# Kernel tuning notes

Measured on AMD Instinct MI355X. Metric: run time of the kernel, lower is better.

The kernel has to match this reference:

```python
import jax, jax.numpy as jnp
import numpy as np

B, L, D, H = 2, 1024, 512, 8
h = D // H            # head_dim = 64
K = H                 # num_eigh must equal num_heads (vmap pairing in conv)
EPS = 1e-5


def _spectral_filters(seq_len: int, k: int) -> np.ndarray:
    # Hankel matrix Z_{ij} = 2 / ((i+j)^3 - (i+j)), top-k eigenvectors scaled by sigma^{1/4}
    e = np.arange(1, seq_len + 1, dtype=np.float64)
    ipj = e[:, None] + e[None, :]
    Z = 2.0 / (ipj ** 3 - ipj)
    sigma, phi = np.linalg.eigh(Z)
    sigma_k = np.clip(sigma[-k:], 1e-9, None)
    return (phi[:, -k:] * sigma_k ** 0.25).astype(np.float32)  # [L, K]


def setup_inputs() -> dict:
    key = jax.random.key(0)
    ks = jax.random.split(key, 8)
    s = 0.02
    return {
        "x": jax.random.normal(ks[0], (B, L, D), jnp.float32),
        "spectral_basis": jnp.asarray(_spectral_filters(L, K)),       # [L, K]
        "wq_w": jax.random.normal(ks[1], (D, D), jnp.float32) * s,
        "wq_b": jnp.zeros((D,), jnp.float32),
        "wk_w": jax.random.normal(ks[2], (D, D), jnp.float32) * s,
        "wk_b": jnp.zeros((D,), jnp.float32),
        "wv_w": jax.random.normal(ks[3], (D, D), jnp.float32) * s,
        "wv_b": jnp.zeros((D,), jnp.float32),
        "wo_w": jax.random.normal(ks[4], (D, D), jnp.float32) * s,
        "wo_b": jnp.zeros((D,), jnp.float32),
        "wg_w": jax.random.normal(ks[5], (h * h,), jnp.float32) * s,  # Linear(h^2 -> 1)
        "wg_b": jnp.zeros((), jnp.float32),
    }


def _causal_fft_conv(u, filt_f, n):
    # u: [B,H,L,h]; filt_f: precomputed rfft of per-head filters [H, F]
    Uf = jnp.fft.rfft(u, n=n, axis=2)                        # [B,H,F,h]
    y = jnp.fft.irfft(Uf * filt_f[None, :, :, None], n=n, axis=2)
    return y[:, :, :L]                                       # truncate full conv -> causal


def reference(x, spectral_basis, wq_w, wq_b, wk_w, wk_b, wv_w, wv_b,
              wo_w, wo_b, wg_w, wg_b):
    # projections -> [B,H,L,h]
    q = (x @ wq_w + wq_b).reshape(B, L, H, h).transpose(0, 2, 1, 3)
    k = (x @ wk_w + wk_b).reshape(B, L, H, h).transpose(0, 2, 1, 3) * h ** (-0.5)
    v = (x @ wv_w + wv_b).reshape(B, L, H, h).transpose(0, 2, 1, 3)

    n = 2 * L
    filt_f = jnp.fft.rfft(spectral_basis.T, n=n, axis=1)     # [H, F] (one filter per head)
    k_conv = _causal_fft_conv(k, filt_f, n)
    v_conv = _causal_fft_conv(v, filt_f, n)

    # gated outer product Z: [B,H,L,h,h]
    Z = jnp.einsum('bhlm,bhln->bhlmn', v_conv, k_conv)
    gate_logits = Z.reshape(B, H, L, h * h) @ wg_w + wg_b    # [B,H,L]
    gates = jax.nn.relu(gate_logits) ** 2 + EPS
    gated_Z = gates[..., None, None] * Z

    # associative scan (additive) over sequence dim
    cumul_gated_Z = jnp.cumsum(gated_Z, axis=2)              # [B,H,L,h,h]
    cumul_gates = jnp.cumsum(gates, axis=2)                  # [B,H,L]
    attn = cumul_gated_Z / (cumul_gates[..., None, None] + EPS)

    # note: original einsum sums over l (and d) independently of s
    ctxt = jnp.einsum('bhsd,bhlde->bhse', q, attn)           # [B,H,L,h]
    norm = jnp.linalg.norm(ctxt, axis=3, keepdims=True)
    unit = ctxt / jnp.maximum(norm, EPS)                     # F.normalize semantics
    out = unit.transpose(0, 2, 1, 3).reshape(B, L, D)
    return out @ wo_w + wo_b
```

## Files before the change

### kernel.cpp

```cpp
#include <hip/hip_runtime.h>
#include <math.h>


typedef __attribute__((ext_vector_type(8))) short short8;
typedef __attribute__((ext_vector_type(4))) float floatx4;

__device__ __forceinline__ unsigned short f2bf(float f) {
    unsigned int u = __float_as_uint(f);
    unsigned int r = (u + 0x7FFFu + ((u >> 16) & 1u)) >> 16;
    return (unsigned short)r;
}

__global__ __launch_bounds__(256) void k_prep(
    const float* __restrict__ x,
    const float* __restrict__ wq, const float* __restrict__ wk,
    const float* __restrict__ wv, const float* __restrict__ wo,
    const float* __restrict__ wg,
    unsigned short* __restrict__ xb,
    unsigned short* __restrict__ wT, unsigned short* __restrict__ woT,
    unsigned short* __restrict__ wgb)
{
    __shared__ float sf[64][65];
    const int blk = blockIdx.x;
    const int tid = threadIdx.x;

    if (blk < 512) {
        const int gid = blk * 256 + tid;
        const float4* x4 = (const float4*)x;
        float4 a = x4[gid*2], b = x4[gid*2+1];
        uint4 o;
        o.x = f2bf(a.x) | ((unsigned)f2bf(a.y) << 16);
        o.y = f2bf(a.z) | ((unsigned)f2bf(a.w) << 16);
        o.z = f2bf(b.x) | ((unsigned)f2bf(b.y) << 16);
        o.w = f2bf(b.z) | ((unsigned)f2bf(b.w) << 16);
        ((uint4*)xb)[gid] = o;
    } else if (blk < 768) {
        const int t = blk - 512;
        const float* src; unsigned short* dst; int n0, c0, k0;
        if (t < 192) {
            int nt = t >> 3, kt = t & 7;
            n0 = nt * 64; k0 = kt * 64;
            int z = n0 >> 9; c0 = n0 & 511;
            src = (z == 0) ? wq : (z == 1) ? wk : wv;
            dst = wT;
        } else {
            int u = t - 192; int nt = u >> 3, kt = u & 7;
            n0 = nt * 64; c0 = n0; k0 = kt * 64;
            src = wo; dst = woT;
        }
        const int rr = tid >> 4, c4 = tid & 15;
        #pragma unroll
        for (int g = 0; g < 4; ++g) {
            int r = g*16 + rr;
            float4 v = *(const float4*)&src[(size_t)(k0 + r)*512 + c0 + c4*4];
            sf[r][c4*4+0]=v.x; sf[r][c4*4+1]=v.y; sf[r][c4*4+2]=v.z; sf[r][c4*4+3]=v.w;
        }
        __syncthreads();
        #pragma unroll
        for (int g = 0; g < 4; ++g) {
            int c = g*16 + rr;
            int kk = c4*4;
            ushort4 o;
            o.x = f2bf(sf[kk+0][c]); o.y = f2bf(sf[kk+1][c]);
            o.z = f2bf(sf[kk+2][c]); o.w = f2bf(sf[kk+3][c]);
            *(ushort4*)&dst[(size_t)(n0 + c)*512 + k0 + kk] = o;
        }
    } else {
        const float4* wg4 = (const float4*)wg;
        for (int i = tid; i < 512; i += 256) {
            float4 a = wg4[i*2], b = wg4[i*2+1];
            uint4 o;
            o.x = f2bf(a.x) | ((unsigned)f2bf(a.y) << 16);
            o.y = f2bf(a.z) | ((unsigned)f2bf(a.w) << 16);
            o.z = f2bf(b.x) | ((unsigned)f2bf(b.y) << 16);
            o.w = f2bf(b.z) | ((unsigned)f2bf(b.w) << 16);
            ((uint4*)wgb)[i] = o;
        }
    }
}

__global__ __launch_bounds__(256) void k_qkv_mfma(
    const unsigned short* __restrict__ xb, const unsigned short* __restrict__ wT,
    const float* __restrict__ bq, const float* __restrict__ bk,
    const float* __restrict__ bv,
    float* __restrict__ qo, unsigned short* __restrict__ ub2)
{
    const int tid = threadIdx.x;
    const int lane = tid & 63, wave = tid >> 6;
    const int q = lane >> 4, ln = lane & 15;
    const int wm = wave * 32;
    const int m0 = blockIdx.y * 128;
    const int n0 = blockIdx.x * 64;

    __shared__ unsigned short As[128*72];
    __shared__ unsigned short Bs[64*72];

    floatx4 acc[2][4];
    #pragma unroll
    for (int i = 0; i < 2; ++i)
        #pragma unroll
        for (int j = 0; j < 4; ++j)
            acc[i][j] = (floatx4){0.f, 0.f, 0.f, 0.f};

    const uint4* Ag = (const uint4*)xb;
    const uint4* Bg = (const uint4*)wT;
    for (int k0 = 0; k0 < 512; k0 += 64) {
        #pragma unroll
        for (int s = 0; s < 4; ++s) {
            int idx = s*256 + tid;
            int r = idx >> 3, cp = idx & 7;
            uint4 va = Ag[(size_t)(m0 + r)*64 + (k0 >> 3) + cp];
            *(uint4*)&As[r*72 + cp*8] = va;
        }
        #pragma unroll
        for (int s = 0; s < 2; ++s) {
            int idx = s*256 + tid;
            int r = idx >> 3, cp = idx & 7;
            uint4 vb = Bg[(size_t)(n0 + r)*64 + (k0 >> 3) + cp];
            *(uint4*)&Bs[r*72 + cp*8] = vb;
        }
        __syncthreads();
        short8 af0[2], af1[2], bf0[4], bf1[4];
        #pragma unroll
        for (int i = 0; i < 2; ++i) {
            af0[i] = *(const short8*)&As[(wm + i*16 + ln)*72 + q*8];
            af1[i] = *(const short8*)&As[(wm + i*16 + ln)*72 + 32 + q*8];
        }
        #pragma unroll
        for (int i = 0; i < 4; ++i) {
            bf0[i] = *(const short8*)&Bs[(i*16 + ln)*72 + q*8];
            bf1[i] = *(const short8*)&Bs[(i*16 + ln)*72 + 32 + q*8];
        }
        #pragma unroll
        for (int mi = 0; mi < 2; ++mi)
            #pragma unroll
            for (int ni = 0; ni < 4; ++ni) {
                acc[mi][ni] = __builtin_amdgcn_mfma_f32_16x16x32_bf16(
                    af0[mi], bf0[ni], acc[mi][ni], 0, 0, 0);
                acc[mi][ni] = __builtin_amdgcn_mfma_f32_16x16x32_bf16(
                    af1[mi], bf1[ni], acc[mi][ni], 0, 0, 0);
            }
        __syncthreads();
    }

    const int z = n0 >> 9;
    if (z == 0) {
        #pragma unroll
        for (int mi = 0; mi < 2; ++mi) {
            #pragma unroll
            for (int ni = 0; ni < 4; ++ni) {
                int c = (n0 + ni*16 + ln) & 511;
                int head = c >> 6, dd = c & 63;
                float bb = bq[c];
                #pragma unroll
                for (int reg = 0; reg < 4; ++reg) {
                    int row = m0 + wm + mi*16 + q*4 + reg;
                    int b = row >> 10, l = row & 1023;
                    qo[(size_t)((b*8 + head)*1024 + l)*64 + dd] =
                        acc[mi][ni][reg] + bb;
                }
            }
        }
    } else {
        const float scale = (z == 1) ? 0.125f : 1.0f;
        const float* bias = (z == 1) ? bk : bv;
        unsigned short* dst = ub2 + (size_t)(z-1) * 16 * 64 * 1024;
        #pragma unroll
        for (int mi = 0; mi < 2; ++mi) {
            #pragma unroll
            for (int ni = 0; ni < 4; ++ni) {
                int c = (n0 + ni*16 + ln) & 511;
                int head = c >> 6, dd = c & 63;
                float bb = bias[c];
                int row0 = m0 + wm + mi*16 + q*4;
                int b = row0 >> 10, l0 = row0 & 1023;
                ushort4 o;
                o.x = f2bf((acc[mi][ni][0] + bb) * scale);
                o.y = f2bf((acc[mi][ni][1] + bb) * scale);
                o.z = f2bf((acc[mi][ni][2] + bb) * scale);
                o.w = f2bf((acc[mi][ni][3] + bb) * scale);
                *(ushort4*)&dst[((size_t)((b*8 + head)*64) + dd)*1024 + l0] = o;
            }
        }
    }
}

__global__ __launch_bounds__(256) void k_conv_gate(
    const float* __restrict__ sb,
    const unsigned short* __restrict__ ub2,
    const unsigned short* __restrict__ wgb, const float* __restrict__ wg_b,
    float* __restrict__ kc, float* __restrict__ vc,
    float* __restrict__ gl)
{
    const int tid = threadIdx.x;
    const int lane = tid & 63, wave = tid >> 6;
    const int q = lane >> 4, ln = lane & 15;
    const int bh  = blockIdx.x, h = bh & 7;
    const int it  = blockIdx.y;
    const int t0  = it * 64;

    __shared__ unsigned short revf[1152];
    __shared__ unsigned short Bk[64*72];
    __shared__ unsigned short Bv[64*72];

    for (int i = tid; i < 1152; i += 256) {
        int d = 1087 - i;
        revf[i] = (d >= 0 && d < 1024) ? f2bf(sb[d*8 + h]) : (unsigned short)0;
    }

    const uint4* Bg = (const uint4*)ub2;
    const size_t bk_base = (size_t)bh * 8192;
    const size_t bv_base = (size_t)(16 + bh) * 8192;

    floatx4 acck[4], accv[4];
    #pragma unroll
    for (int i = 0; i < 4; ++i) {
        acck[i] = (floatx4){0.f,0.f,0.f,0.f};
        accv[i] = (floatx4){0.f,0.f,0.f,0.f};
    }

    const int kend = t0 + 64;
    const int arow = 1087 - t0 - (wave*16 + ln);
    for (int k0 = 0; k0 < kend; k0 += 64) {
        #pragma unroll
        for (int s = 0; s < 2; ++s) {
            int idx = s*256 + tid;
            int r = idx >> 3, cp = idx & 7;
            *(uint4*)&Bk[r*72 + cp*8] = Bg[bk_base + (size_t)r*128 + (k0 >> 3) + cp];
            *(uint4*)&Bv[r*72 + cp*8] = Bg[bv_base + (size_t)r*128 + (k0 >> 3) + cp];
        }
        __syncthreads();
        const int ab = arow + k0 + q*8;
        short8 a0, a1;
        #pragma unroll
        for (int j = 0; j < 8; ++j) {
            a0[j] = (short)revf[ab + j];
            a1[j] = (short)revf[ab + 32 + j];
        }
        #pragma unroll
        for (int ni = 0; ni < 4; ++ni) {
            short8 kb0 = *(const short8*)&Bk[(ni*16 + ln)*72 + q*8];
            short8 kb1 = *(const short8*)&Bk[(ni*16 + ln)*72 + 32 + q*8];
            short8 vb0 = *(const short8*)&Bv[(ni*16 + ln)*72 + q*8];
            short8 vb1 = *(const short8*)&Bv[(ni*16 + ln)*72 + 32 + q*8];
            acck[ni] = __builtin_amdgcn_mfma_f32_16x16x32_bf16(a0, kb0, acck[ni], 0, 0, 0);
            acck[ni] = __builtin_amdgcn_mfma_f32_16x16x32_bf16(a1, kb1, acck[ni], 0, 0, 0);
            accv[ni] = __builtin_amdgcn_mfma_f32_16x16x32_bf16(a0, vb0, accv[ni], 0, 0, 0);
            accv[ni] = __builtin_amdgcn_mfma_f32_16x16x32_bf16(a1, vb1, accv[ni], 0, 0, 0);
        }
        __syncthreads();
    }

    float* kdst = kc + (size_t)bh * 65536;
    float* vdst = vc + (size_t)bh * 65536;
    #pragma unroll
    for (int ni = 0; ni < 4; ++ni)
        #pragma unroll
        for (int reg = 0; reg < 4; ++reg) {
            int row = wave*16 + q*4 + reg;
            int grow = t0 + row;
            kdst[(size_t)grow*64 + ni*16 + ln] = acck[ni][reg];
            vdst[(size_t)grow*64 + ni*16 + ln] = accv[ni][reg];
            Bk[row*72 + ni*16 + ln] = f2bf(acck[ni][reg]);
        }
    {
        const uint4* Wg = (const uint4*)wgb;
        #pragma unroll
        for (int s = 0; s < 2; ++s) {
            int idx = s*256 + tid;
            int r = idx >> 3, cp = idx & 7;
            *(uint4*)&Bv[r*72 + cp*8] = Wg[r*8 + cp];
        }
    }
    __syncthreads();

    floatx4 T[4];
    #pragma unroll
    for (int mt = 0; mt < 4; ++mt) T[mt] = (floatx4){0.f,0.f,0.f,0.f};
    #pragma unroll
    for (int k0g = 0; k0g < 64; k0g += 32) {
        short8 a = *(const short8*)&Bk[(wave*16 + ln)*72 + k0g + q*8];
        #pragma unroll
        for (int mt = 0; mt < 4; ++mt) {
            short8 b = *(const short8*)&Bv[(mt*16 + ln)*72 + k0g + q*8];
            T[mt] = __builtin_amdgcn_mfma_f32_16x16x32_bf16(a, b, T[mt], 0, 0, 0);
        }
    }

    float part[4] = {0.f, 0.f, 0.f, 0.f};
    #pragma unroll
    for (int mt = 0; mt < 4; ++mt)
        #pragma unroll
        for (int reg = 0; reg < 4; ++reg)
            part[reg] += T[mt][reg] * accv[mt][reg];
    #pragma unroll
    for (int reg = 0; reg < 4; ++reg) {
        part[reg] += __shfl_xor(part[reg], 1);
        part[reg] += __shfl_xor(part[reg], 2);
        part[reg] += __shfl_xor(part[reg], 4);
        part[reg] += __shfl_xor(part[reg], 8);
    }
    if (ln == 0) {
        const float wgbias = wg_b[0];
        #pragma unroll
        for (int reg = 0; reg < 4; ++reg) {
            int l = t0 + wave*16 + q*4 + reg;
            float s = part[reg] + wgbias;
            float rr = fmaxf(s, 0.0f);
            gl[bh*1024 + l] = rr*rr + 1e-5f;
        }
    }
}

__global__ __launch_bounds__(256) void k_amat(
    const float* __restrict__ kc, const float* __restrict__ vc,
    const float* __restrict__ gl, float* __restrict__ apart)
{
    const int tid = threadIdx.x, tx = tid & 15, ty = tid >> 4;
    const int lane = tid & 63, wave = tid >> 6;
    const int bh = blockIdx.x, slc = blockIdx.y;
    const float* kb = kc + (size_t)bh * 65536;
    const float* vb = vc + (size_t)bh * 65536;

    __shared__ float scanA[4], scanB[4];
    __shared__ float wfull[1024];
    __shared__ __align__(16) float vs[16][68];
    __shared__ __align__(16) float ks2[16][68];

    {
        const float4 g4 = ((const float4*)(gl + bh*1024))[tid];
        float g[4] = {g4.x, g4.y, g4.z, g4.w};
        float p[4];
        p[0]=g[0]; p[1]=p[0]+g[1]; p[2]=p[1]+g[2]; p[3]=p[2]+g[3];
        float x = p[3];
        #pragma unroll
        for (int off = 1; off < 64; off <<= 1) {
            float t = __shfl_up(x, off);
            if (lane >= off) x += t;
        }
        if (lane == 63) scanA[wave] = x;
        __syncthreads();
        float wb = 0.f;
        #pragma unroll
        for (int wv = 0; wv < 4; ++wv) wb += (wv < wave) ? scanA[wv] : 0.f;
        const float base = wb + x - p[3];
        float r[4], pr[4];
        #pragma unroll
        for (int u = 0; u < 4; ++u) r[u] = 1.0f / (base + p[u] + 1e-5f);
        pr[0]=r[0]; pr[1]=pr[0]+r[1]; pr[2]=pr[1]+r[2]; pr[3]=pr[2]+r[3];
        float y = pr[3];
        #pragma unroll
        for (int off = 1; off < 64; off <<= 1) {
            float t = __shfl_up(y, off);
            if (lane >= off) y += t;
        }
        if (lane == 63) scanB[wave] = y;
        __syncthreads();
        float rb = 0.f, Rtot = 0.f;
        #pragma unroll
        for (int wv = 0; wv < 4; ++wv) {
            rb   += (wv < wave) ? scanB[wv] : 0.f;
            Rtot += scanB[wv];
        }
        const float baser = rb + y - pr[3];
        wfull[tid*4+0] = g[0] * (Rtot - (baser + pr[0] - pr[3]) - pr[3] + pr[3] - (pr[0] - r[0]) - r[0] + r[0]);
        wfull[tid*4+0] = g[0] * (Rtot - (baser + pr[0]) + r[0]);
        wfull[tid*4+1] = g[1] * (Rtot - (baser + pr[1]) + r[1]);
        wfull[tid*4+2] = g[2] * (Rtot - (baser + pr[2]) + r[2]);
        wfull[tid*4+3] = g[3] * (Rtot - (baser + pr[3]) + r[3]);
    }
    __syncthreads();

    float acc[4][4] = {};
    const float4* k4 = (const float4*)kb;
    const float4* v4 = (const float4*)vb;
    for (int j0 = slc*64; j0 < slc*64 + 64; j0 += 16) {
        {
            int r = tid >> 4, c4 = tid & 15;
            *(float4*)&vs[r][c4*4]  = v4[(size_t)(j0 + r)*16 + c4];
            *(float4*)&ks2[r][c4*4] = k4[(size_t)(j0 + r)*16 + c4];
        }
        __syncthreads();
        #pragma unroll
        for (int jj = 0; jj < 16; ++jj) {
            float wj = wfull[j0 + jj];
            float a[4];
            a[0] = vs[jj][ty*4+0]*wj; a[1] = vs[jj][ty*4+1]*wj;
            a[2] = vs[jj][ty*4+2]*wj; a[3] = vs[jj][ty*4+3]*wj;
            float4 b4 = *(const float4*)&ks2[jj][tx*4];
            float bb[4] = {b4.x, b4.y, b4.z, b4.w};
            #pragma unroll
            for (int ii = 0; ii < 4; ++ii)
                #pragma unroll
                for (int jc = 0; jc < 4; ++jc)
                    acc[ii][jc] += a[ii] * bb[jc];
        }
        __syncthreads();
    }
    float* ap = apart + (size_t)(slc*16 + bh) * 4096;
    #pragma unroll
    for (int i = 0; i < 4; ++i) {
        float4 o = { acc[i][0], acc[i][1], acc[i][2], acc[i][3] };
        *(float4*)&ap[(ty*4+i)*64 + tx*4] = o;
    }
}

__global__ __launch_bounds__(256) void k_ctxt(
    const float* __restrict__ q, const float* __restrict__ apart,
    unsigned short* __restrict__ ub)
{
    const int tid = threadIdx.x, tx = tid & 15, ty = tid >> 4;
    const int l0 = blockIdx.x * 64;
    const int bh = blockIdx.y;
    const float* qb = q + (size_t)bh * 65536;

    __shared__ __align__(16) float qs[64][20];
    __shared__ __align__(16) float As[16][68];
    float acc[4][4] = {};
    const float4* q4 = (const float4*)qb;
    const float4* a4 = (const float4*)apart;
    for (int d0 = 0; d0 < 64; d0 += 16) {
        {
            int r = tid >> 2, c4 = tid & 3;
            float4 t = q4[(size_t)(l0 + r)*16 + (d0 >> 2) + c4];
            *(float4*)&qs[r][c4*4] = t;
        }
        {
            int r = tid >> 4, c4 = tid & 15;
            size_t o = (size_t)(d0 + r)*16 + c4;
            float4 t = a4[(size_t)(0*16 + bh)*1024 + o];
            #pragma unroll
            for (int s = 1; s < 16; ++s) {
                float4 u = a4[(size_t)(s*16 + bh)*1024 + o];
                t.x += u.x; t.y += u.y; t.z += u.z; t.w += u.w;
            }
            *(float4*)&As[r][c4*4] = t;
        }
        __syncthreads();
        float qreg[4][16];
        #pragma unroll
        for (int i = 0; i < 4; ++i)
            #pragma unroll
            for (int c = 0; c < 4; ++c) {
                float4 t = *(const float4*)&qs[ty*4+i][c*4];
                qreg[i][c*4+0] = t.x; qreg[i][c*4+1] = t.y;
                qreg[i][c*4+2] = t.z; qreg[i][c*4+3] = t.w;
            }
        #pragma unroll
        for (int dd = 0; dd < 16; ++dd) {
            float4 b4 = *(const float4*)&As[dd][tx*4];
            float bb[4] = {b4.x, b4.y, b4.z, b4.w};
            #pragma unroll
            for (int ii = 0; ii < 4; ++ii)
                #pragma unroll
                for (int jj = 0; jj < 4; ++jj)
                    acc[ii][jj] += qreg[ii][dd] * bb[jj];
        }
        __syncthreads();
    }
    __shared__ float red[64][17];
    __shared__ float nrm[64];
    #pragma unroll
    for (int i = 0; i < 4; ++i) {
        red[ty*4+i][tx] = acc[i][0]*acc[i][0] + acc[i][1]*acc[i][1]
                        + acc[i][2]*acc[i][2] + acc[i][3]*acc[i][3];
    }
    __syncthreads();
    if (tid < 64) {
        float s = 0.0f;
        #pragma unroll
        for (int t = 0; t < 16; ++t) s += red[tid][t];
        nrm[tid] = fmaxf(sqrtf(s), 1e-5f);
    }
    __syncthreads();
    const int b = bh >> 3, hd = bh & 7;
    #pragma unroll
    for (int i = 0; i < 4; ++i) {
        int lr = ty*4 + i;
        float inv = 1.0f / nrm[lr];
        ushort4 o;
        o.x = f2bf(acc[i][0]*inv); o.y = f2bf(acc[i][1]*inv);
        o.z = f2bf(acc[i][2]*inv); o.w = f2bf(acc[i][3]*inv);
        *(ushort4*)&ub[(size_t)(b*1024 + l0 + lr)*512 + hd*64 + tx*4] = o;
    }
}

__global__ __launch_bounds__(256) void k_out_mfma(
    const unsigned short* __restrict__ ub, const unsigned short* __restrict__ woT,
    const float* __restrict__ bo, float* __restrict__ out)
{
    const int tid = threadIdx.x;
    const int lane = tid & 63, wave = tid >> 6;
    const int q = lane >> 4, ln = lane & 15;
    const int wm = wave * 32;
    const int m0 = blockIdx.y * 128;
    const int n0 = blockIdx.x * 64;

    __shared__ unsigned short As[128*72];
    __shared__ unsigned short Bs[64*72];

    floatx4 acc[2][4];
    #pragma unroll
    for (int i = 0; i < 2; ++i)
        #pragma unroll
        for (int j = 0; j < 4; ++j)
            acc[i][j] = (floatx4){0.f, 0.f, 0.f, 0.f};

    const uint4* Ag = (const uint4*)ub;
    const uint4* Bg = (const uint4*)woT;
    for (int k0 = 0; k0 < 512; k0 += 64) {
        #pragma unroll
        for (int s = 0; s < 4; ++s) {
            int idx = s*256 + tid;
            int r = idx >> 3, cp = idx & 7;
            uint4 va = Ag[(size_t)(m0 + r)*64 + (k0 >> 3) + cp];
            *(uint4*)&As[r*72 + cp*8] = va;
        }
        #pragma unroll
        for (int s = 0; s < 2; ++s) {
            int idx = s*256 + tid;
            int r = idx >> 3, cp = idx & 7;
            uint4 vb = Bg[(size_t)(n0 + r)*64 + (k0 >> 3) + cp];
            *(uint4*)&Bs[r*72 + cp*8] = vb;
        }
        __syncthreads();
        short8 af0[2], af1[2], bf0[4], bf1[4];
        #pragma unroll
        for (int i = 0; i < 2; ++i) {
            af0[i] = *(const short8*)&As[(wm + i*16 + ln)*72 + q*8];
            af1[i] = *(const short8*)&As[(wm + i*16 + ln)*72 + 32 + q*8];
        }
        #pragma unroll
        for (int i = 0; i < 4; ++i) {
            bf0[i] = *(const short8*)&Bs[(i*16 + ln)*72 + q*8];
            bf1[i] = *(const short8*)&Bs[(i*16 + ln)*72 + 32 + q*8];
        }
        #pragma unroll
        for (int mi = 0; mi < 2; ++mi)
            #pragma unroll
            for (int ni = 0; ni < 4; ++ni) {
                acc[mi][ni] = __builtin_amdgcn_mfma_f32_16x16x32_bf16(
                    af0[mi], bf0[ni], acc[mi][ni], 0, 0, 0);
                acc[mi][ni] = __builtin_amdgcn_mfma_f32_16x16x32_bf16(
                    af1[mi], bf1[ni], acc[mi][ni], 0, 0, 0);
            }
        __syncthreads();
    }

    #pragma unroll
    for (int mi = 0; mi < 2; ++mi) {
        #pragma unroll
        for (int ni = 0; ni < 4; ++ni) {
            int gcol = n0 + ni*16 + ln;
            float bb = bo[gcol];
            #pragma unroll
            for (int reg = 0; reg < 4; ++reg) {
                int row = m0 + wm + mi*16 + q*4 + reg;
                out[(size_t)row*512 + gcol] = acc[mi][ni][reg] + bb;
            }
        }
    }
}

extern "C" void kernel_launch(void* const* d_in, const int* in_sizes, int n_in,
                              void* d_out, int out_size, void* d_ws, size_t ws_size,
                              hipStream_t stream)
{
    const float* x   = (const float*)d_in[0];
    const float* sb  = (const float*)d_in[1];
    const float* wq  = (const float*)d_in[2];
    const float* bq  = (const float*)d_in[3];
    const float* wk  = (const float*)d_in[4];
    const float* bk  = (const float*)d_in[5];
    const float* wv  = (const float*)d_in[6];
    const float* bv  = (const float*)d_in[7];
    const float* wo  = (const float*)d_in[8];
    const float* bo  = (const float*)d_in[9];
    const float* wg  = (const float*)d_in[10];
    const float* wgb = (const float*)d_in[11];
    float* out = (float*)d_out;
    float* ws  = (float*)d_ws;

    float* Q   = ws;
    float* KC  = ws + 1048576;
    float* VC  = ws + 2*1048576;
    float* GL  = ws + 3*1048576;
    float* AP  = GL + 16384;
    float* fp  = AP + 1048576;
    unsigned short* XB  = (unsigned short*)fp;
    unsigned short* WT  = XB  + 1048576;
    unsigned short* WOT = WT  + 786432;
    unsigned short* UB  = WOT + 262144;
    unsigned short* UB2 = UB  + 1048576;
    unsigned short* WGB = UB2 + 2097152;

    k_prep     <<<dim3(769),    256, 0, stream>>>(x, wq, wk, wv, wo, wg,
                                                  XB, WT, WOT, WGB);
    k_qkv_mfma <<<dim3(24, 16), 256, 0, stream>>>(XB, WT, bq, bk, bv, Q, UB2);
    k_conv_gate<<<dim3(16, 16), 256, 0, stream>>>(sb, UB2, WGB, wgb, KC, VC, GL);
    k_amat     <<<dim3(16, 16), 256, 0, stream>>>(KC, VC, GL, AP);
    k_ctxt     <<<dim3(16, 16), 256, 0, stream>>>(Q, AP, UB);
    k_out_mfma <<<dim3(8, 16),  256, 0, stream>>>(UB, WOT, bo, out);
}
```

Baseline: 143.7 us.

## Fuse all stages into one persistent kernel with atomic grid barriers

Replaces the six separate kernel launches with one persistent 256-block kernel. Stages are separated by software grid barriers built on atomic counters, and a memset resets the counters before launch. The conv and gate stage now keeps the k/v convolution results on chip instead of writing KC/VC to global memory, and the output GEMM uses smaller 64x64 tiles to spread across all 256 blocks. This is meant to remove launch gaps and intermediate traffic. In exchange, all blocks must be co-resident for the barriers to work, the spinning adds overhead, and some stages lose parallelism.

```diff
diff --git a/kernel.cpp b/kernel.cpp
--- a/kernel.cpp
+++ b/kernel.cpp
@@ -11,383 +11,380 @@
     return (unsigned short)r;
 }
 
-__global__ __launch_bounds__(256) void k_prep(
-    const float* __restrict__ x,
+__device__ __forceinline__ void gsync(unsigned int* cnt, unsigned target) {
+    __syncthreads();
+    if (threadIdx.x == 0) {
+        __threadfence();
+        __hip_atomic_fetch_add(cnt, 1u, __ATOMIC_RELAXED,
+                               __HIP_MEMORY_SCOPE_AGENT);
+        while (__hip_atomic_load(cnt, __ATOMIC_RELAXED,
+                                 __HIP_MEMORY_SCOPE_AGENT) < target) {
+            __builtin_amdgcn_s_sleep(2);
+        }
+        __threadfence();
+    }
+    __syncthreads();
+}
+
+__global__ __launch_bounds__(256, 1) void k_mega(
+    const float* __restrict__ x, const float* __restrict__ sb,
     const float* __restrict__ wq, const float* __restrict__ wk,
     const float* __restrict__ wv, const float* __restrict__ wo,
-    const float* __restrict__ wg,
-    unsigned short* __restrict__ xb,
-    unsigned short* __restrict__ wT, unsigned short* __restrict__ woT,
-    unsigned short* __restrict__ wgb)
+    const float* __restrict__ wgw,
+    const float* __restrict__ bq, const float* __restrict__ bk,
+    const float* __restrict__ bv, const float* __restrict__ bo,
+    const float* __restrict__ wgbias,
+    unsigned short* __restrict__ XB, unsigned short* __restrict__ WT,
+    unsigned short* __restrict__ WOT, unsigned short* __restrict__ WGB,
+    float* __restrict__ Qb, unsigned short* __restrict__ UB2,
+    float* __restrict__ GL, float* __restrict__ AP,
+    float* __restrict__ AF, unsigned short* __restrict__ UB,
+    float* __restrict__ out,
+    unsigned int* __restrict__ CNT)
 {
-    __shared__ float sf[64][65];
     const int blk = blockIdx.x;
     const int tid = threadIdx.x;
-
-    if (blk < 512) {
-        const int gid = blk * 256 + tid;
+    const int lane = tid & 63, wave = tid >> 6;
+    const int qd = lane >> 4, ln = lane & 15;
+    const int tx = tid & 15, ty = tid >> 4;
+
+    __shared__ __align__(16) unsigned char arena[55552];
+
+    {
+        float (*sf)[65] = (float(*)[65])arena;
         const float4* x4 = (const float4*)x;
-        float4 a = x4[gid*2], b = x4[gid*2+1];
-        uint4 o;
-        o.x = f2bf(a.x) | ((unsigned)f2bf(a.y) << 16);
-        o.y = f2bf(a.z) | ((unsigned)f2bf(a.w) << 16);
-        o.z = f2bf(b.x) | ((unsigned)f2bf(b.y) << 16);
-        o.w = f2bf(b.z) | ((unsigned)f2bf(b.w) << 16);
-        ((uint4*)xb)[gid] = o;
-    } else if (blk < 768) {
-        const int t = blk - 512;
-        const float* src; unsigned short* dst; int n0, c0, k0;
-        if (t < 192) {
-            int nt = t >> 3, kt = t & 7;
-            n0 = nt * 64; k0 = kt * 64;
-            int z = n0 >> 9; c0 = n0 & 511;
-            src = (z == 0) ? wq : (z == 1) ? wk : wv;
-            dst = wT;
-        } else {
-            int u = t - 192; int nt = u >> 3, kt = u & 7;
-            n0 = nt * 64; c0 = n0; k0 = kt * 64;
-            src = wo; dst = woT;
-        }
-        const int rr = tid >> 4, c4 = tid & 15;
-        #pragma unroll
-        for (int g = 0; g < 4; ++g) {
-            int r = g*16 + rr;
-            float4 v = *(const float4*)&src[(size_t)(k0 + r)*512 + c0 + c4*4];
-            sf[r][c4*4+0]=v.x; sf[r][c4*4+1]=v.y; sf[r][c4*4+2]=v.z; sf[r][c4*4+3]=v.w;
-        }
-        __syncthreads();
-        #pragma unroll
-        for (int g = 0; g < 4; ++g) {
-            int c = g*16 + rr;
-            int kk = c4*4;
-            ushort4 o;
-            o.x = f2bf(sf[kk+0][c]); o.y = f2bf(sf[kk+1][c]);
-            o.z = f2bf(sf[kk+2][c]); o.w = f2bf(sf[kk+3][c]);
-            *(ushort4*)&dst[(size_t)(n0 + c)*512 + k0 + kk] = o;
-        }
-    } else {
-        const float4* wg4 = (const float4*)wg;
-        for (int i = tid; i < 512; i += 256) {
-            float4 a = wg4[i*2], b = wg4[i*2+1];
+        #pragma unroll
+        for (int u = 0; u < 2; ++u) {
+            int gid = (blk + u*256) * 256 + tid;
+            float4 a = x4[gid*2], b = x4[gid*2+1];
             uint4 o;
             o.x = f2bf(a.x) | ((unsigned)f2bf(a.y) << 16);
             o.y = f2bf(a.z) | ((unsigned)f2bf(a.w) << 16);
             o.z = f2bf(b.x) | ((unsigned)f2bf(b.y) << 16);
             o.w = f2bf(b.z) | ((unsigned)f2bf(b.w) << 16);
-            ((uint4*)wgb)[i] = o;
-        }
-    }
-}
-
-__global__ __launch_bounds__(256) void k_qkv_mfma(
-    const unsigned short* __restrict__ xb, const unsigned short* __restrict__ wT,
-    const float* __restrict__ bq, const float* __restrict__ bk,
-    const float* __restrict__ bv,
-    float* __restrict__ qo, unsigned short* __restrict__ ub2)
-{
-    const int tid = threadIdx.x;
-    const int lane = tid & 63, wave = tid >> 6;
-    const int q = lane >> 4, ln = lane & 15;
-    const int wm = wave * 32;
-    const int m0 = blockIdx.y * 128;
-    const int n0 = blockIdx.x * 64;
-
-    __shared__ unsigned short As[128*72];
-    __shared__ unsigned short Bs[64*72];
-
-    floatx4 acc[2][4];
-    #pragma unroll
-    for (int i = 0; i < 2; ++i)
-        #pragma unroll
-        for (int j = 0; j < 4; ++j)
-            acc[i][j] = (floatx4){0.f, 0.f, 0.f, 0.f};
-
-    const uint4* Ag = (const uint4*)xb;
-    const uint4* Bg = (const uint4*)wT;
-    for (int k0 = 0; k0 < 512; k0 += 64) {
-        #pragma unroll
-        for (int s = 0; s < 4; ++s) {
-            int idx = s*256 + tid;
-            int r = idx >> 3, cp = idx & 7;
-            uint4 va = Ag[(size_t)(m0 + r)*64 + (k0 >> 3) + cp];
-            *(uint4*)&As[r*72 + cp*8] = va;
-        }
-        #pragma unroll
-        for (int s = 0; s < 2; ++s) {
-            int idx = s*256 + tid;
-            int r = idx >> 3, cp = idx & 7;
-            uint4 vb = Bg[(size_t)(n0 + r)*64 + (k0 >> 3) + cp];
-            *(uint4*)&Bs[r*72 + cp*8] = vb;
+            ((uint4*)XB)[gid] = o;
+        }
+        {
+            const int t = blk;
+            const float* src; unsigned short* dst; int n0p, c0, k0p;
+            if (t < 192) {
+                int nt = t >> 3, kt = t & 7;
+                n0p = nt * 64; k0p = kt * 64;
+                int z = n0p >> 9; c0 = n0p & 511;
+                src = (z == 0) ? wq : (z == 1) ? wk : wv;
+                dst = WT;
+            } else {
+                int u = t - 192; int nt = u >> 3, kt = u & 7;
+                n0p = nt * 64; c0 = n0p; k0p = kt * 64;
+                src = wo; dst = WOT;
+            }
+            const int rr = tid >> 4, c4 = tid & 15;
+            #pragma unroll
+            for (int g = 0; g < 4; ++g) {
+                int r = g*16 + rr;
+                float4 v = *(const float4*)&src[(size_t)(k0p + r)*512 + c0 + c4*4];
+                sf[r][c4*4+0]=v.x; sf[r][c4*4+1]=v.y; sf[r][c4*4+2]=v.z; sf[r][c4*4+3]=v.w;
+            }
+            __syncthreads();
+            #pragma unroll
+            for (int g = 0; g < 4; ++g) {
+                int c = g*16 + rr;
+                int kk = c4*4;
+                ushort4 o;
+                o.x = f2bf(sf[kk+0][c]); o.y = f2bf(sf[kk+1][c]);
+                o.z = f2bf(sf[kk+2][c]); o.w = f2bf(sf[kk+3][c]);
+                *(ushort4*)&dst[(size_t)(n0p + c)*512 + k0p + kk] = o;
+            }
+        }
+        if (blk == 0) {
+            const float4* wg4 = (const float4*)wgw;
+            for (int i = tid; i < 512; i += 256) {
+                float4 a = wg4[i*2], b = wg4[i*2+1];
+                uint4 o;
+                o.x = f2bf(a.x) | ((unsigned)f2bf(a.y) << 16);
+                o.y = f2bf(a.z) | ((unsigned)f2bf(a.w) << 16);
+                o.z = f2bf(b.x) | ((unsigned)f2bf(b.y) << 16);
+                o.w = f2bf(b.z) | ((unsigned)f2bf(b.w) << 16);
+                ((uint4*)WGB)[i] = o;
+            }
+        }
+    }
+    gsync(CNT + 0, 256);
+
+    {
+        unsigned short* As = (unsigned short*)arena;
+        unsigned short* Bs = (unsigned short*)(arena + 18432);
+        const int wm = wave * 32;
+        const uint4* Ag = (const uint4*)XB;
+        const uint4* Bg = (const uint4*)WT;
+        for (int t = blk; t < 384; t += 256) {
+            const int m0 = (t / 24) * 128;
+            const int n0 = (t % 24) * 64;
+
+            floatx4 acc[2][4];
+            #pragma unroll
+            for (int i = 0; i < 2; ++i)
+                #pragma unroll
+                for (int j = 0; j < 4; ++j)
+                    acc[i][j] = (floatx4){0.f, 0.f, 0.f, 0.f};
+
+            for (int k0 = 0; k0 < 512; k0 += 64) {
+                #pragma unroll
+                for (int s = 0; s < 4; ++s) {
+                    int idx = s*256 + tid;
+                    int r = idx >> 3, cp = idx & 7;
+                    uint4 va = Ag[(size_t)(m0 + r)*64 + (k0 >> 3) + cp];
+                    *(uint4*)&As[r*72 + cp*8] = va;
+                }
+                #pragma unroll
+                for (int s = 0; s < 2; ++s) {
+                    int idx = s*256 + tid;
+                    int r = idx >> 3, cp = idx & 7;
+                    uint4 vb = Bg[(size_t)(n0 + r)*64 + (k0 >> 3) + cp];
+                    *(uint4*)&Bs[r*72 + cp*8] = vb;
+                }
+                __syncthreads();
+                short8 af0[2], af1[2], bf0[4], bf1[4];
+                #pragma unroll
+                for (int i = 0; i < 2; ++i) {
+                    af0[i] = *(const short8*)&As[(wm + i*16 + ln)*72 + qd*8];
+                    af1[i] = *(const short8*)&As[(wm + i*16 + ln)*72 + 32 + qd*8];
+                }
+                #pragma unroll
+                for (int i = 0; i < 4; ++i) {
+                    bf0[i] = *(const short8*)&Bs[(i*16 + ln)*72 + qd*8];
+                    bf1[i] = *(const short8*)&Bs[(i*16 + ln)*72 + 32 + qd*8];
+                }
+                #pragma unroll
+                for (int mi = 0; mi < 2; ++mi)
+                    #pragma unroll
+                    for (int ni = 0; ni < 4; ++ni) {
+                        acc[mi][ni] = __builtin_amdgcn_mfma_f32_16x16x32_bf16(
+                            af0[mi], bf0[ni], acc[mi][ni], 0, 0, 0);
+                        acc[mi][ni] = __builtin_amdgcn_mfma_f32_16x16x32_bf16(
+                            af1[mi], bf1[ni], acc[mi][ni], 0, 0, 0);
+                    }
+                __syncthreads();
+            }
+
+            const int z = n0 >> 9;
+            if (z == 0) {
+                #pragma unroll
+                for (int mi = 0; mi < 2; ++mi) {
+                    #pragma unroll
+                    for (int ni = 0; ni < 4; ++ni) {
+                        int c = (n0 + ni*16 + ln) & 511;
+                        int head = c >> 6, dd = c & 63;
+                        float bb = bq[c];
+                        #pragma unroll
+                        for (int reg = 0; reg < 4; ++reg) {
+                            int row = m0 + wm + mi*16 + qd*4 + reg;
+                            int b = row >> 10, l = row & 1023;
+                            Qb[(size_t)((b*8 + head)*1024 + l)*64 + dd] =
+                                acc[mi][ni][reg] + bb;
+                        }
+                    }
+                }
+            } else {
+                const float scale = (z == 1) ? 0.125f : 1.0f;
+                const float* bias = (z == 1) ? bk : bv;
+                unsigned short* dst = UB2 + (size_t)(z-1) * 16 * 64 * 1024;
+                #pragma unroll
+                for (int mi = 0; mi < 2; ++mi) {
+                    #pragma unroll
+                    for (int ni = 0; ni < 4; ++ni) {
+                        int c = (n0 + ni*16 + ln) & 511;
+                        int head = c >> 6, dd = c & 63;
+                        float bb = bias[c];
+                        int row0 = m0 + wm + mi*16 + qd*4;
+                        int b = row0 >> 10, l0 = row0 & 1023;
+                        ushort4 o;
+                        o.x = f2bf((acc[mi][ni][0] + bb) * scale);
+                        o.y = f2bf((acc[mi][ni][1] + bb) * scale);
+                        o.z = f2bf((acc[mi][ni][2] + bb) * scale);
+                        o.w = f2bf((acc[mi][ni][3] + bb) * scale);
+                        *(ushort4*)&dst[((size_t)((b*8 + head)*64) + dd)*1024 + l0] = o;
+                    }
+                }
+            }
+        }
+    }
+    gsync(CNT + 1, 256);
+
+    {
+        float (*kts)[68] = (float(*)[68])arena;
+        float (*vts)[68] = (float(*)[68])(arena + 17408);
+        unsigned short* revf = (unsigned short*)(arena + 34816);
+        unsigned short* Bk = (unsigned short*)(arena + 37120);
+        unsigned short* Bv = (unsigned short*)(arena + 46336);
+        const int bh = blk & 15, h = bh & 7;
+        const int it = blk >> 4, t0 = it * 64;
+
+        for (int i = tid; i < 1152; i += 256) {
+            int d = 1087 - i;
+            revf[i] = (d >= 0 && d < 1024) ? f2bf(sb[d*8 + h]) : (unsigned short)0;
+        }
+
+        const uint4* Bg = (const uint4*)UB2;
+        const size_t bk_base = (size_t)bh * 8192;
+        const size_t bv_base = (size_t)(16 + bh) * 8192;
+
+        floatx4 acck[4], accv[4];
+        #pragma unroll
+        for (int i = 0; i < 4; ++i) {
+            acck[i] = (floatx4){0.f,0.f,0.f,0.f};
+            accv[i] = (floatx4){0.f,0.f,0.f,0.f};
+        }
+
+        const int kend = t0 + 64;
+        const int arow = 1087 - t0 - (wave*16 + ln);
+        for (int k0 = 0; k0 < kend; k0 += 64) {
+            #pragma unroll
+            for (int s = 0; s < 2; ++s) {
+                int idx = s*256 + tid;
+                int r = idx >> 3, cp = idx & 7;
+                *(uint4*)&Bk[r*72 + cp*8] = Bg[bk_base + (size_t)r*128 + (k0 >> 3) + cp];
+                *(uint4*)&Bv[r*72 + cp*8] = Bg[bv_base + (size_t)r*128 + (k0 >> 3) + cp];
+            }
+            __syncthreads();
+            const int ab = arow + k0 + qd*8;
+            short8 a0, a1;
+            #pragma unroll
+            for (int j = 0; j < 8; ++j) {
+                a0[j] = (short)revf[ab + j];
+                a1[j] = (short)revf[ab + 32 + j];
+            }
+            #pragma unroll
+            for (int ni = 0; ni < 4; ++ni) {
+                short8 kb0 = *(const short8*)&Bk[(ni*16 + ln)*72 + qd*8];
+                short8 kb1 = *(const short8*)&Bk[(ni*16 + ln)*72 + 32 + qd*8];
+                short8 vb0 = *(const short8*)&Bv[(ni*16 + ln)*72 + qd*8];
+                short8 vb1 = *(const short8*)&Bv[(ni*16 + ln)*72 + 32 + qd*8];
+                acck[ni] = __builtin_amdgcn_mfma_f32_16x16x32_bf16(a0, kb0, acck[ni], 0, 0, 0);
+                acck[ni] = __builtin_amdgcn_mfma_f32_16x16x32_bf16(a1, kb1, acck[ni], 0, 0, 0);
+                accv[ni] = __builtin_amdgcn_mfma_f32_16x16x32_bf16(a0, vb0, accv[ni], 0, 0, 0);
+                accv[ni] = __builtin_amdgcn_mfma_f32_16x16x32_bf16(a1, vb1, accv[ni], 0, 0, 0);
+            }
+            __syncthreads();
+        }
+
+        #pragma unroll
+        for (int ni = 0; ni < 4; ++ni)
+            #pragma unroll
+            for (int reg = 0; reg < 4; ++reg) {
+                int row = wave*16 + qd*4 + reg;
+                kts[row][ni*16 + ln] = acck[ni][reg];
+                vts[row][ni*16 + ln] = accv[ni][reg];
+                Bk[row*72 + ni*16 + ln] = f2bf(acck[ni][reg]);
+            }
+        {
+            const uint4* Wg = (const uint4*)WGB;
+            #pragma unroll
+            for (int s = 0; s < 2; ++s) {
+                int idx = s*256 + tid;
+                int r = idx >> 3, cp = idx & 7;
+                *(uint4*)&Bv[r*72 + cp*8] = Wg[r*8 + cp];
+            }
         }
         __syncthreads();
-        short8 af0[2], af1[2], bf0[4], bf1[4];
-        #pragma unroll
-        for (int i = 0; i < 2; ++i) {
-            af0[i] = *(const short8*)&As[(wm + i*16 + ln)*72 + q*8];
-            af1[i] = *(const short8*)&As[(wm + i*16 + ln)*72 + 32 + q*8];
-        }
-        #pragma unroll
-        for (int i = 0; i < 4; ++i) {
-            bf0[i] = *(const short8*)&Bs[(i*16 + ln)*72 + q*8];
-            bf1[i] = *(const short8*)&Bs[(i*16 + ln)*72 + 32 + q*8];
-        }
-        #pragma unroll
-        for (int mi = 0; mi < 2; ++mi)
-            #pragma unroll
-            for (int ni = 0; ni < 4; ++ni) {
-                acc[mi][ni] = __builtin_amdgcn_mfma_f32_16x16x32_bf16(
-                    af0[mi], bf0[ni], acc[mi][ni], 0, 0, 0);
-                acc[mi][ni] = __builtin_amdgcn_mfma_f32_16x16x32_bf16(
-                    af1[mi], bf1[ni], acc[mi][ni], 0, 0, 0);
-            }
+
+        floatx4 T[4];
+        #pragma unroll
+        for (int mt = 0; mt < 4; ++mt) T[mt] = (floatx4){0.f,0.f,0.f,0.f};
+        #pragma unroll
+        for (int k0g = 0; k0g < 64; k0g += 32) {
+            short8 a = *(const short8*)&Bk[(wave*16 + ln)*72 + k0g + qd*8];
+            #pragma unroll
+            for (int mt = 0; mt < 4; ++mt) {
+                short8 b = *(const short8*)&Bv[(mt*16 + ln)*72 + k0g + qd*8];
+                T[mt] = __builtin_amdgcn_mfma_f32_16x16x32_bf16(a, b, T[mt], 0, 0, 0);
+            }
+        }
+
+        float part[4] = {0.f, 0.f, 0.f, 0.f};
+        #pragma unroll
+        for (int mt = 0; mt < 4; ++mt)
+            #pragma unroll
+            for (int reg = 0; reg < 4; ++reg)
+                part[reg] += T[mt][reg] * accv[mt][reg];
+        #pragma unroll
+        for (int reg = 0; reg < 4; ++reg) {
+            part[reg] += __shfl_xor(part[reg], 1);
+            part[reg] += __shfl_xor(part[reg], 2);
+            part[reg] += __shfl_xor(part[reg], 4);
+            part[reg] += __shfl_xor(part[reg], 8);
+        }
+        if (ln == 0) {
+            const float wb0 = wgbias[0];
+            #pragma unroll
+            for (int reg = 0; reg < 4; ++reg) {
+                int l = t0 + wave*16 + qd*4 + reg;
+                float s = part[reg] + wb0;
+                float rr = fmaxf(s, 0.0f);
+                GL[bh*1024 + l] = rr*rr + 1e-5f;
+            }
+        }
+    }
+    gsync(CNT + 2, 256);
+
+    {
+        float (*kts)[68] = (float(*)[68])arena;
+        float (*vts)[68] = (float(*)[68])(arena + 17408);
+        float* wfull = (float*)(arena + 34816);
+        float* scanA = (float*)(arena + 38912);
+        float* scanB = (float*)(arena + 38928);
+        const int bh = blk & 15, it = blk >> 4, t0 = it * 64;
+
+        {
+            const float4 g4 = ((const float4*)(GL + bh*1024))[tid];
+            float g[4] = {g4.x, g4.y, g4.z, g4.w};
+            float p[4];
+            p[0]=g[0]; p[1]=p[0]+g[1]; p[2]=p[1]+g[2]; p[3]=p[2]+g[3];
+            float xs = p[3];
+            #pragma unroll
+            for (int off = 1; off < 64; off <<= 1) {
+                float t = __shfl_up(xs, off);
+                if (lane >= off) xs += t;
+            }
+            if (lane == 63) scanA[wave] = xs;
+            __syncthreads();
+            float wb = 0.f;
+            #pragma unroll
+            for (int wv2 = 0; wv2 < 4; ++wv2) wb += (wv2 < wave) ? scanA[wv2] : 0.f;
+            const float base = wb + xs - p[3];
+            float r[4], pr[4];
+            #pragma unroll
+            for (int u = 0; u < 4; ++u) r[u] = 1.0f / (base + p[u] + 1e-5f);
+            pr[0]=r[0]; pr[1]=pr[0]+r[1]; pr[2]=pr[1]+r[2]; pr[3]=pr[2]+r[3];
+            float y = pr[3];
+            #pragma unroll
+            for (int off = 1; off < 64; off <<= 1) {
+                float t = __shfl_up(y, off);
+                if (lane >= off) y += t;
+            }
+            if (lane == 63) scanB[wave] = y;
+            __syncthreads();
+            float rb = 0.f, Rtot = 0.f;
+            #pragma unroll
+            for (int wv2 = 0; wv2 < 4; ++wv2) {
+                rb   += (wv2 < wave) ? scanB[wv2] : 0.f;
+                Rtot += scanB[wv2];
+            }
+            const float baser = rb + y - pr[3];
+            wfull[tid*4+0] = g[0] * (Rtot - (baser + pr[0]) + r[0]);
+            wfull[tid*4+1] = g[1] * (Rtot - (baser + pr[1]) + r[1]);
+            wfull[tid*4+2] = g[2] * (Rtot - (baser + pr[2]) + r[2]);
+            wfull[tid*4+3] = g[3] * (Rtot - (baser + pr[3]) + r[3]);
+        }
         __syncthreads();
-    }
-
-    const int z = n0 >> 9;
-    if (z == 0) {
-        #pragma unroll
-        for (int mi = 0; mi < 2; ++mi) {
-            #pragma unroll
-            for (int ni = 0; ni < 4; ++ni) {
-                int c = (n0 + ni*16 + ln) & 511;
-                int head = c >> 6, dd = c & 63;
-                float bb = bq[c];
-                #pragma unroll
-                for (int reg = 0; reg < 4; ++reg) {
-                    int row = m0 + wm + mi*16 + q*4 + reg;
-                    int b = row >> 10, l = row & 1023;
-                    qo[(size_t)((b*8 + head)*1024 + l)*64 + dd] =
-                        acc[mi][ni][reg] + bb;
-                }
-            }
-        }
-    } else {
-        const float scale = (z == 1) ? 0.125f : 1.0f;
-        const float* bias = (z == 1) ? bk : bv;
-        unsigned short* dst = ub2 + (size_t)(z-1) * 16 * 64 * 1024;
-        #pragma unroll
-        for (int mi = 0; mi < 2; ++mi) {
-            #pragma unroll
-            for (int ni = 0; ni < 4; ++ni) {
-                int c = (n0 + ni*16 + ln) & 511;
-                int head = c >> 6, dd = c & 63;
-                float bb = bias[c];
-                int row0 = m0 + wm + mi*16 + q*4;
-                int b = row0 >> 10, l0 = row0 & 1023;
-                ushort4 o;
-                o.x = f2bf((acc[mi][ni][0] + bb) * scale);
-                o.y = f2bf((acc[mi][ni][1] + bb) * scale);
-                o.z = f2bf((acc[mi][ni][2] + bb) * scale);
-                o.w = f2bf((acc[mi][ni][3] + bb) * scale);
-                *(ushort4*)&dst[((size_t)((b*8 + head)*64) + dd)*1024 + l0] = o;
-            }
-        }
-    }
-}
-
-__global__ __launch_bounds__(256) void k_conv_gate(
-    const float* __restrict__ sb,
-    const unsigned short* __restrict__ ub2,
-    const unsigned short* __restrict__ wgb, const float* __restrict__ wg_b,
-    float* __restrict__ kc, float* __restrict__ vc,
-    float* __restrict__ gl)
-{
-    const int tid = threadIdx.x;
-    const int lane = tid & 63, wave = tid >> 6;
-    const int q = lane >> 4, ln = lane & 15;
-    const int bh  = blockIdx.x, h = bh & 7;
-    const int it  = blockIdx.y;
-    const int t0  = it * 64;
-
-    __shared__ unsigned short revf[1152];
-    __shared__ unsigned short Bk[64*72];
-    __shared__ unsigned short Bv[64*72];
-
-    for (int i = tid; i < 1152; i += 256) {
-        int d = 1087 - i;
-        revf[i] = (d >= 0 && d < 1024) ? f2bf(sb[d*8 + h]) : (unsigned short)0;
-    }
-
-    const uint4* Bg = (const uint4*)ub2;
-    const size_t bk_base = (size_t)bh * 8192;
-    const size_t bv_base = (size_t)(16 + bh) * 8192;
-
-    floatx4 acck[4], accv[4];
-    #pragma unroll
-    for (int i = 0; i < 4; ++i) {
-        acck[i] = (floatx4){0.f,0.f,0.f,0.f};
-        accv[i] = (floatx4){0.f,0.f,0.f,0.f};
-    }
-
-    const int kend = t0 + 64;
-    const int arow = 1087 - t0 - (wave*16 + ln);
-    for (int k0 = 0; k0 < kend; k0 += 64) {
-        #pragma unroll
-        for (int s = 0; s < 2; ++s) {
-            int idx = s*256 + tid;
-            int r = idx >> 3, cp = idx & 7;
-            *(uint4*)&Bk[r*72 + cp*8] = Bg[bk_base + (size_t)r*128 + (k0 >> 3) + cp];
-            *(uint4*)&Bv[r*72 + cp*8] = Bg[bv_base + (size_t)r*128 + (k0 >> 3) + cp];
-        }
-        __syncthreads();
-        const int ab = arow + k0 + q*8;
-        short8 a0, a1;
-        #pragma unroll
-        for (int j = 0; j < 8; ++j) {
-            a0[j] = (short)revf[ab + j];
-            a1[j] = (short)revf[ab + 32 + j];
-        }
-        #pragma unroll
-        for (int ni = 0; ni < 4; ++ni) {
-            short8 kb0 = *(const short8*)&Bk[(ni*16 + ln)*72 + q*8];
-            short8 kb1 = *(const short8*)&Bk[(ni*16 + ln)*72 + 32 + q*8];
-            short8 vb0 = *(const short8*)&Bv[(ni*16 + ln)*72 + q*8];
-            short8 vb1 = *(const short8*)&Bv[(ni*16 + ln)*72 + 32 + q*8];
-            acck[ni] = __builtin_amdgcn_mfma_f32_16x16x32_bf16(a0, kb0, acck[ni], 0, 0, 0);
-            acck[ni] = __builtin_amdgcn_mfma_f32_16x16x32_bf16(a1, kb1, acck[ni], 0, 0, 0);
-            accv[ni] = __builtin_amdgcn_mfma_f32_16x16x32_bf16(a0, vb0, accv[ni], 0, 0, 0);
-            accv[ni] = __builtin_amdgcn_mfma_f32_16x16x32_bf16(a1, vb1, accv[ni], 0, 0, 0);
-        }
-        __syncthreads();
-    }
-
-    float* kdst = kc + (size_t)bh * 65536;
-    float* vdst = vc + (size_t)bh * 65536;
-    #pragma unroll
-    for (int ni = 0; ni < 4; ++ni)
-        #pragma unroll
-        for (int reg = 0; reg < 4; ++reg) {
-            int row = wave*16 + q*4 + reg;
-            int grow = t0 + row;
-            kdst[(size_t)grow*64 + ni*16 + ln] = acck[ni][reg];
-            vdst[(size_t)grow*64 + ni*16 + ln] = accv[ni][reg];
-            Bk[row*72 + ni*16 + ln] = f2bf(acck[ni][reg]);
-        }
-    {
-        const uint4* Wg = (const uint4*)wgb;
-        #pragma unroll
-        for (int s = 0; s < 2; ++s) {
-            int idx = s*256 + tid;
-            int r = idx >> 3, cp = idx & 7;
-            *(uint4*)&Bv[r*72 + cp*8] = Wg[r*8 + cp];
-        }
-    }
-    __syncthreads();
-
-    floatx4 T[4];
-    #pragma unroll
-    for (int mt = 0; mt < 4; ++mt) T[mt] = (floatx4){0.f,0.f,0.f,0.f};
-    #pragma unroll
-    for (int k0g = 0; k0g < 64; k0g += 32) {
-        short8 a = *(const short8*)&Bk[(wave*16 + ln)*72 + k0g + q*8];
-        #pragma unroll
-        for (int mt = 0; mt < 4; ++mt) {
-            short8 b = *(const short8*)&Bv[(mt*16 + ln)*72 + k0g + q*8];
-            T[mt] = __builtin_amdgcn_mfma_f32_16x16x32_bf16(a, b, T[mt], 0, 0, 0);
-        }
-    }
-
-    float part[4] = {0.f, 0.f, 0.f, 0.f};
-    #pragma unroll
-    for (int mt = 0; mt < 4; ++mt)
-        #pragma unroll
-        for (int reg = 0; reg < 4; ++reg)
-            part[reg] += T[mt][reg] * accv[mt][reg];
-    #pragma unroll
-    for (int reg = 0; reg < 4; ++reg) {
-        part[reg] += __shfl_xor(part[reg], 1);
-        part[reg] += __shfl_xor(part[reg], 2);
-        part[reg] += __shfl_xor(part[reg], 4);
-        part[reg] += __shfl_xor(part[reg], 8);
-    }
-    if (ln == 0) {
-        const float wgbias = wg_b[0];
-        #pragma unroll
-        for (int reg = 0; reg < 4; ++reg) {
-            int l = t0 + wave*16 + q*4 + reg;
-            float s = part[reg] + wgbias;
-            float rr = fmaxf(s, 0.0f);
-            gl[bh*1024 + l] = rr*rr + 1e-5f;
-        }
-    }
-}
-
-__global__ __launch_bounds__(256) void k_amat(
-    const float* __restrict__ kc, const float* __restrict__ vc,
-    const float* __restrict__ gl, float* __restrict__ apart)
-{
-    const int tid = threadIdx.x, tx = tid & 15, ty = tid >> 4;
-    const int lane = tid & 63, wave = tid >> 6;
-    const int bh = blockIdx.x, slc = blockIdx.y;
-    const float* kb = kc + (size_t)bh * 65536;
-    const float* vb = vc + (size_t)bh * 65536;
-
-    __shared__ float scanA[4], scanB[4];
-    __shared__ float wfull[1024];
-    __shared__ __align__(16) float vs[16][68];
-    __shared__ __align__(16) float ks2[16][68];
-
-    {
-        const float4 g4 = ((const float4*)(gl + bh*1024))[tid];
-        float g[4] = {g4.x, g4.y, g4.z, g4.w};
-        float p[4];
-        p[0]=g[0]; p[1]=p[0]+g[1]; p[2]=p[1]+g[2]; p[3]=p[2]+g[3];
-        float x = p[3];
-        #pragma unroll
-        for (int off = 1; off < 64; off <<= 1) {
-            float t = __shfl_up(x, off);
-            if (lane >= off) x += t;
-        }
-        if (lane == 63) scanA[wave] = x;
-        __syncthreads();
-        float wb = 0.f;
-        #pragma unroll
-        for (int wv = 0; wv < 4; ++wv) wb += (wv < wave) ? scanA[wv] : 0.f;
-        const float base = wb + x - p[3];
-        float r[4], pr[4];
-        #pragma unroll
-        for (int u = 0; u < 4; ++u) r[u] = 1.0f / (base + p[u] + 1e-5f);
-        pr[0]=r[0]; pr[1]=pr[0]+r[1]; pr[2]=pr[1]+r[2]; pr[3]=pr[2]+r[3];
-        float y = pr[3];
-        #pragma unroll
-        for (int off = 1; off < 64; off <<= 1) {
-            float t = __shfl_up(y, off);
-            if (lane >= off) y += t;
-        }
-        if (lane == 63) scanB[wave] = y;
-        __syncthreads();
-        float rb = 0.f, Rtot = 0.f;
-        #pragma unroll
-        for (int wv = 0; wv < 4; ++wv) {
-            rb   += (wv < wave) ? scanB[wv] : 0.f;
-            Rtot += scanB[wv];
-        }
-        const float baser = rb + y - pr[3];
-        wfull[tid*4+0] = g[0] * (Rtot - (baser + pr[0] - pr[3]) - pr[3] + pr[3] - (pr[0] - r[0]) - r[0] + r[0]);
-        wfull[tid*4+0] = g[0] * (Rtot - (baser + pr[0]) + r[0]);
-        wfull[tid*4+1] = g[1] * (Rtot - (baser + pr[1]) + r[1]);
-        wfull[tid*4+2] = g[2] * (Rtot - (baser + pr[2]) + r[2]);
-        wfull[tid*4+3] = g[3] * (Rtot - (baser + pr[3]) + r[3]);
-    }
-    __syncthreads();
-
-    float acc[4][4] = {};
-    const float4* k4 = (const float4*)kb;
-    const float4* v4 = (const float4*)vb;
-    for (int j0 = slc*64; j0 < slc*64 + 64; j0 += 16) {
-        {
-            int r = tid >> 4, c4 = tid & 15;
-            *(float4*)&vs[r][c4*4]  = v4[(size_t)(j0 + r)*16 + c4];
-            *(float4*)&ks2[r][c4*4] = k4[(size_t)(j0 + r)*16 + c4];
-        }
-        __syncthreads();
-        #pragma unroll
-        for (int jj = 0; jj < 16; ++jj) {
-            float wj = wfull[j0 + jj];
-            float a[4];
-            a[0] = vs[jj][ty*4+0]*wj; a[1] = vs[jj][ty*4+1]*wj;
-            a[2] = vs[jj][ty*4+2]*wj; a[3] = vs[jj][ty*4+3]*wj;
-            float4 b4 = *(const float4*)&ks2[jj][tx*4];
+
+        float acc[4][4] = {};
+        #pragma unroll 16
+        for (int jj = 0; jj < 64; ++jj) {
+            float wj = wfull[t0 + jj];
+            float4 av = *(const float4*)&vts[jj][ty*4];
+            float a[4] = { av.x*wj, av.y*wj, av.z*wj, av.w*wj };
+            float4 b4 = *(const float4*)&kts[jj][tx*4];
             float bb[4] = {b4.x, b4.y, b4.z, b4.w};
             #pragma unroll
             for (int ii = 0; ii < 4; ++ii)
@@ -395,168 +392,137 @@
                 for (int jc = 0; jc < 4; ++jc)
                     acc[ii][jc] += a[ii] * bb[jc];
         }
+        float* ap = AP + (size_t)(it*16 + bh) * 4096;
+        #pragma unroll
+        for (int i = 0; i < 4; ++i) {
+            float4 o = { acc[i][0], acc[i][1], acc[i][2], acc[i][3] };
+            *(float4*)&ap[(ty*4+i)*64 + tx*4] = o;
+        }
+    }
+    gsync(CNT + 3, 256);
+
+    {
+        const int bh = blk >> 4, p = blk & 15;
+        int idx = p*256 + tid;
+        float s = 0.f;
+        #pragma unroll
+        for (int sl = 0; sl < 16; ++sl)
+            s += AP[(size_t)(sl*16 + bh)*4096 + idx];
+        AF[bh*4096 + idx] = s;
+    }
+    gsync(CNT + 4, 256);
+
+    {
+        float (*qs)[20]  = (float(*)[20])arena;
+        float (*As16)[68] = (float(*)[68])(arena + 5120);
+        float (*red)[17] = (float(*)[17])(arena + 9472);
+        float* nrm = (float*)(arena + 13824);
+        const int l0 = (blk >> 4) * 64;
+        const int bh = blk & 15;
+        const float* qb = Qb + (size_t)bh * 65536;
+
+        float acc[4][4] = {};
+        const float4* q4 = (const float4*)qb;
+        for (int d0 = 0; d0 < 64; d0 += 16) {
+            {
+                int r = tid >> 2, c4 = tid & 3;
+                float4 t = q4[(size_t)(l0 + r)*16 + (d0 >> 2) + c4];
+                *(float4*)&qs[r][c4*4] = t;
+            }
+            {
+                int r = tid >> 4, c4 = tid & 15;
+                float4 t = ((const float4*)AF)[(size_t)bh*1024 + (size_t)(d0 + r)*16 + c4];
+                *(float4*)&As16[r][c4*4] = t;
+            }
+            __syncthreads();
+            float qreg[4][16];
+            #pragma unroll
+            for (int i = 0; i < 4; ++i)
+                #pragma unroll
+                for (int c = 0; c < 4; ++c) {
+                    float4 t = *(const float4*)&qs[ty*4+i][c*4];
+                    qreg[i][c*4+0] = t.x; qreg[i][c*4+1] = t.y;
+                    qreg[i][c*4+2] = t.z; qreg[i][c*4+3] = t.w;
+                }
+            #pragma unroll
+            for (int dd = 0; dd < 16; ++dd) {
+                float4 b4 = *(const float4*)&As16[dd][tx*4];
+                float bb[4] = {b4.x, b4.y, b4.z, b4.w};
+                #pragma unroll
+                for (int ii = 0; ii < 4; ++ii)
+                    #pragma unroll
+                    for (int jj = 0; jj < 4; ++jj)
+                        acc[ii][jj] += qreg[ii][dd] * bb[jj];
+            }
+            __syncthreads();
+        }
+        #pragma unroll
+        for (int i = 0; i < 4; ++i) {
+            red[ty*4+i][tx] = acc[i][0]*acc[i][0] + acc[i][1]*acc[i][1]
+                            + acc[i][2]*acc[i][2] + acc[i][3]*acc[i][3];
+        }
         __syncthreads();
-    }
-    float* ap = apart + (size_t)(slc*16 + bh) * 4096;
-    #pragma unroll
-    for (int i = 0; i < 4; ++i) {
-        float4 o = { acc[i][0], acc[i][1], acc[i][2], acc[i][3] };
-        *(float4*)&ap[(ty*4+i)*64 + tx*4] = o;
-    }
-}
-
-__global__ __launch_bounds__(256) void k_ctxt(
-    const float* __restrict__ q, const float* __restrict__ apart,
-    unsigned short* __restrict__ ub)
-{
-    const int tid = threadIdx.x, tx = tid & 15, ty = tid >> 4;
-    const int l0 = blockIdx.x * 64;
-    const int bh = blockIdx.y;
-    const float* qb = q + (size_t)bh * 65536;
-
-    __shared__ __align__(16) float qs[64][20];
-    __shared__ __align__(16) float As[16][68];
-    float acc[4][4] = {};
-    const float4* q4 = (const float4*)qb;
-    const float4* a4 = (const float4*)apart;
-    for (int d0 = 0; d0 < 64; d0 += 16) {
-        {
-            int r = tid >> 2, c4 = tid & 3;
-            float4 t = q4[(size_t)(l0 + r)*16 + (d0 >> 2) + c4];
-            *(float4*)&qs[r][c4*4] = t;
-        }
-        {
-            int r = tid >> 4, c4 = tid & 15;
-            size_t o = (size_t)(d0 + r)*16 + c4;
-            float4 t = a4[(size_t)(0*16 + bh)*1024 + o];
-            #pragma unroll
-            for (int s = 1; s < 16; ++s) {
-                float4 u = a4[(size_t)(s*16 + bh)*1024 + o];
-                t.x += u.x; t.y += u.y; t.z += u.z; t.w += u.w;
-            }
-            *(float4*)&As[r][c4*4] = t;
+        if (tid < 64) {
+            float s = 0.0f;
+            #pragma unroll
+            for (int t = 0; t < 16; ++t) s += red[tid][t];
+            nrm[tid] = fmaxf(sqrtf(s), 1e-5f);
         }
         __syncthreads();
-        float qreg[4][16];
-        #pragma unroll
-        for (int i = 0; i < 4; ++i)
-            #pragma unroll
-            for (int c = 0; c < 4; ++c) {
-                float4 t = *(const float4*)&qs[ty*4+i][c*4];
-                qreg[i][c*4+0] = t.x; qreg[i][c*4+1] = t.y;
-                qreg[i][c*4+2] = t.z; qreg[i][c*4+3] = t.w;
-            }
-        #pragma unroll
-        for (int dd = 0; dd < 16; ++dd) {
-            float4 b4 = *(const float4*)&As[dd][tx*4];
-            float bb[4] = {b4.x, b4.y, b4.z, b4.w};
-            #pragma unroll
-            for (int ii = 0; ii < 4; ++ii)
-                #pragma unroll
-                for (int jj = 0; jj < 4; ++jj)
-                    acc[ii][jj] += qreg[ii][dd] * bb[jj];
-        }
-        __syncthreads();
-    }
-    __shared__ float red[64][17];
-    __shared__ float nrm[64];
-    #pragma unroll
-    for (int i = 0; i < 4; ++i) {
-        red[ty*4+i][tx] = acc[i][0]*acc[i][0] + acc[i][1]*acc[i][1]
-                        + acc[i][2]*acc[i][2] + acc[i][3]*acc[i][3];
-    }
-    __syncthreads();
-    if (tid < 64) {
-        float s = 0.0f;
-        #pragma unroll
-        for (int t = 0; t < 16; ++t) s += red[tid][t];
-        nrm[tid] = fmaxf(sqrtf(s), 1e-5f);
-    }
-    __syncthreads();
-    const int b = bh >> 3, hd = bh & 7;
-    #pragma unroll
-    for (int i = 0; i < 4; ++i) {
-        int lr = ty*4 + i;
-        float inv = 1.0f / nrm[lr];
-        ushort4 o;
-        o.x = f2bf(acc[i][0]*inv); o.y = f2bf(acc[i][1]*inv);
-        o.z = f2bf(acc[i][2]*inv); o.w = f2bf(acc[i][3]*inv);
-        *(ushort4*)&ub[(size_t)(b*1024 + l0 + lr)*512 + hd*64 + tx*4] = o;
-    }
-}
-
-__global__ __launch_bounds__(256) void k_out_mfma(
-    const unsigned short* __restrict__ ub, const unsigned short* __restrict__ woT,
-    const float* __restrict__ bo, float* __restrict__ out)
-{
-    const int tid = threadIdx.x;
-    const int lane = tid & 63, wave = tid >> 6;
-    const int q = lane >> 4, ln = lane & 15;
-    const int wm = wave * 32;
-    const int m0 = blockIdx.y * 128;
-    const int n0 = blockIdx.x * 64;
-
-    __shared__ unsigned short As[128*72];
-    __shared__ unsigned short Bs[64*72];
-
-    floatx4 acc[2][4];
-    #pragma unroll
-    for (int i = 0; i < 2; ++i)
-        #pragma unroll
-        for (int j = 0; j < 4; ++j)
-            acc[i][j] = (floatx4){0.f, 0.f, 0.f, 0.f};
-
-    const uint4* Ag = (const uint4*)ub;
-    const uint4* Bg = (const uint4*)woT;
-    for (int k0 = 0; k0 < 512; k0 += 64) {
-        #pragma unroll
-        for (int s = 0; s < 4; ++s) {
-            int idx = s*256 + tid;
-            int r = idx >> 3, cp = idx & 7;
-            uint4 va = Ag[(size_t)(m0 + r)*64 + (k0 >> 3) + cp];
-            *(uint4*)&As[r*72 + cp*8] = va;
-        }
-        #pragma unroll
-        for (int s = 0; s < 2; ++s) {
-            int idx = s*256 + tid;
-            int r = idx >> 3, cp = idx & 7;
-            uint4 vb = Bg[(size_t)(n0 + r)*64 + (k0 >> 3) + cp];
-            *(uint4*)&Bs[r*72 + cp*8] = vb;
-        }
-        __syncthreads();
-        short8 af0[2], af1[2], bf0[4], bf1[4];
-        #pragma unroll
-        for (int i = 0; i < 2; ++i) {
-            af0[i] = *(const short8*)&As[(wm + i*16 + ln)*72 + q*8];
-            af1[i] = *(const short8*)&As[(wm + i*16 + ln)*72 + 32 + q*8];
-        }
+        const int b = bh >> 3, hd = bh & 7;
         #pragma unroll
         for (int i = 0; i < 4; ++i) {
-            bf0[i] = *(const short8*)&Bs[(i*16 + ln)*72 + q*8];
-            bf1[i] = *(const short8*)&Bs[(i*16 + ln)*72 + 32 + q*8];
-        }
-        #pragma unroll
-        for (int mi = 0; mi < 2; ++mi)
+            int lr = ty*4 + i;
+            float inv = 1.0f / nrm[lr];
+            ushort4 o;
+            o.x = f2bf(acc[i][0]*inv); o.y = f2bf(acc[i][1]*inv);
+            o.z = f2bf(acc[i][2]*inv); o.w = f2bf(acc[i][3]*inv);
+            *(ushort4*)&UB[(size_t)(b*1024 + l0 + lr)*512 + hd*64 + tx*4] = o;
+        }
+    }
+    gsync(CNT + 5, 256);
+
+    {
+        unsigned short* As = (unsigned short*)arena;
+        unsigned short* Bs = (unsigned short*)(arena + 9216);
+        const int m0 = (blk >> 3) * 64;
+        const int n0 = (blk & 7) * 64;
+
+        floatx4 acc[4];
+        #pragma unroll
+        for (int i = 0; i < 4; ++i) acc[i] = (floatx4){0.f,0.f,0.f,0.f};
+
+        const uint4* Ag = (const uint4*)UB;
+        const uint4* Bg = (const uint4*)WOT;
+        for (int k0 = 0; k0 < 512; k0 += 64) {
+            #pragma unroll
+            for (int s = 0; s < 2; ++s) {
+                int idx = s*256 + tid;
+                int r = idx >> 3, cp = idx & 7;
+                *(uint4*)&As[r*72 + cp*8] = Ag[(size_t)(m0 + r)*64 + (k0 >> 3) + cp];
+                *(uint4*)&Bs[r*72 + cp*8] = Bg[(size_t)(n0 + r)*64 + (k0 >> 3) + cp];
+            }
+            __syncthreads();
+            short8 af0 = *(const short8*)&As[(wave*16 + ln)*72 + qd*8];
+            short8 af1 = *(const short8*)&As[(wave*16 + ln)*72 + 32 + qd*8];
             #pragma unroll
             for (int ni = 0; ni < 4; ++ni) {
-                acc[mi][ni] = __builtin_amdgcn_mfma_f32_16x16x32_bf16(
-                    af0[mi], bf0[ni], acc[mi][ni], 0, 0, 0);
-                acc[mi][ni] = __builtin_amdgcn_mfma_f32_16x16x32_bf16(
-                    af1[mi], bf1[ni], acc[mi][ni], 0, 0, 0);
-            }
-        __syncthreads();
-    }
-
-    #pragma unroll
-    for (int mi = 0; mi < 2; ++mi) {
+                short8 bf0 = *(const short8*)&Bs[(ni*16 + ln)*72 + qd*8];
+                short8 bf1 = *(const short8*)&Bs[(ni*16 + ln)*72 + 32 + qd*8];
+                acc[ni] = __builtin_amdgcn_mfma_f32_16x16x32_bf16(af0, bf0, acc[ni], 0, 0, 0);
+                acc[ni] = __builtin_amdgcn_mfma_f32_16x16x32_bf16(af1, bf1, acc[ni], 0, 0, 0);
+            }
+            __syncthreads();
+        }
+
         #pragma unroll
         for (int ni = 0; ni < 4; ++ni) {
             int gcol = n0 + ni*16 + ln;
             float bb = bo[gcol];
             #pragma unroll
             for (int reg = 0; reg < 4; ++reg) {
-                int row = m0 + wm + mi*16 + q*4 + reg;
-                out[(size_t)row*512 + gcol] = acc[mi][ni][reg] + bb;
+                int row = m0 + wave*16 + qd*4 + reg;
+                out[(size_t)row*512 + gcol] = acc[ni][reg] + bb;
             }
         }
     }
@@ -581,12 +547,12 @@
     float* out = (float*)d_out;
     float* ws  = (float*)d_ws;
 
-    float* Q   = ws;
-    float* KC  = ws + 1048576;
-    float* VC  = ws + 2*1048576;
-    float* GL  = ws + 3*1048576;
+    unsigned int* CNT = (unsigned int*)ws;
+    float* Qb  = ws + 64;
+    float* GL  = Qb + 1048576;
     float* AP  = GL + 16384;
-    float* fp  = AP + 1048576;
+    float* AF  = AP + 1048576;
+    float* fp  = AF + 65536;
     unsigned short* XB  = (unsigned short*)fp;
     unsigned short* WT  = XB  + 1048576;
     unsigned short* WOT = WT  + 786432;
@@ -594,11 +560,8 @@
     unsigned short* UB2 = UB  + 1048576;
     unsigned short* WGB = UB2 + 2097152;
 
-    k_prep     <<<dim3(769),    256, 0, stream>>>(x, wq, wk, wv, wo, wg,
-                                                  XB, WT, WOT, WGB);
-    k_qkv_mfma <<<dim3(24, 16), 256, 0, stream>>>(XB, WT, bq, bk, bv, Q, UB2);
-    k_conv_gate<<<dim3(16, 16), 256, 0, stream>>>(sb, UB2, WGB, wgb, KC, VC, GL);
-    k_amat     <<<dim3(16, 16), 256, 0, stream>>>(KC, VC, GL, AP);
-    k_ctxt     <<<dim3(16, 16), 256, 0, stream>>>(Q, AP, UB);
-    k_out_mfma <<<dim3(8, 16),  256, 0, stream>>>(UB, WOT, bo, out);
+    hipMemsetAsync(CNT, 0, 64, stream);
+    k_mega<<<dim3(256), dim3(256), 0, stream>>>(
+        x, sb, wq, wk, wv, wo, wg, bq, bk, bv, bo, wgb,
+        XB, WT, WOT, WGB, Qb, UB2, GL, AP, AF, UB, out, CNT);
 }
```

New measurement: 264.4 us. +83.9%, slower.
